# Kernel tuning notes

Measured on AMD Instinct MI355X. Metric: run time of the kernel, lower is better.

## Reference

```python
import jax, jax.numpy as jnp
import numpy as np

N_EMB = 1024
HEAD_SIZE = 64
BLOCK_SIZE = 2048
B, T = 8, 2048


def setup_inputs() -> dict:
    key = jax.random.key(0)
    kx, kq, kk, kv = jax.random.split(key, 4)
    scale = 1.0 / (N_EMB ** 0.5)
    x = jax.random.normal(kx, (B, T, N_EMB), dtype=jnp.float32)
    Wq = jax.random.uniform(kq, (N_EMB, HEAD_SIZE), dtype=jnp.float32) * scale
    Wk = jax.random.uniform(kk, (N_EMB, HEAD_SIZE), dtype=jnp.float32) * scale
    Wv = jax.random.uniform(kv, (N_EMB, HEAD_SIZE), dtype=jnp.float32) * scale
    return {"x": x, "Wq": Wq, "Wk": Wk, "Wv": Wv}


def reference(x, Wq, Wk, Wv):
    # Faithful to Head.__call__ with is_training=False.
    # NOTE: original code applies NO 1/sqrt(head_size) scaling to the scores.
    Bt, Tt, _ = x.shape
    q = x @ Wq                      # (B, T, H)
    k = x @ Wk                      # (B, T, H)
    v = x @ Wv                      # (B, T, H)
    wei = jnp.einsum('bth,bsh->bts', q, k)  # (B, T, T)
    causal = jnp.tril(jnp.ones((Tt, Tt), dtype=bool))
    wei = jnp.where(causal, wei, -jnp.inf)
    wei = jax.nn.softmax(wei, axis=-1)
    out = jnp.einsum('bts,bsh->bth', wei, v)  # (B, T, H)
    return out
```

## Files before the change

kernel.cpp:

```cpp
#include <hip/hip_runtime.h>
#include <hip/hip_bf16.h>

#define BB 8
#define TT 2048
#define EE 1024
#define HH 64

typedef __attribute__((ext_vector_type(8))) short short8;
typedef __attribute__((ext_vector_type(4))) float f32x4;

__device__ inline f32x4 mfma_16x16x32(short8 a, short8 b, f32x4 c) {
  return __builtin_amdgcn_mfma_f32_16x16x32_bf16(a, b, c, 0, 0, 0);
}

__device__ inline void gload_lds16(const __hip_bfloat16* g, __hip_bfloat16* l) {
  __builtin_amdgcn_global_load_lds((const __attribute__((address_space(1))) void*)g,
                                   (__attribute__((address_space(3))) void*)l,
                                   16, 0, 0);
}

__device__ inline short f2bf(float f) {
  __hip_bfloat16 h = __float2bfloat16(f);
  return *reinterpret_cast<short*>(&h);
}
__device__ inline float bf2f(short s) {
  __hip_bfloat16 h = *reinterpret_cast<__hip_bfloat16*>(&s);
  return __bfloat162float(h);
}

#define WAIT_LGKM0() __builtin_amdgcn_s_waitcnt(0xC07F)

__global__ void prep_w(const float* __restrict__ Wq, const float* __restrict__ Wk,
                       const float* __restrict__ Wv,
                       __hip_bfloat16* __restrict__ Wthi,
                       __hip_bfloat16* __restrict__ Wtlo) {
  const int n = blockIdx.x;
  const int m = n >> 6;
  const int h = n & 63;
  const float* W = (m == 0) ? Wq : (m == 1) ? Wk : Wv;
  const int e0 = threadIdx.x * 4;
#pragma unroll
  for (int j = 0; j < 4; ++j) {
    const float w = W[(e0 + j) * 64 + h];
    const __hip_bfloat16 hi = __float2bfloat16(w);
    Wthi[n * 1024 + e0 + j] = hi;
    Wtlo[n * 1024 + e0 + j] = __float2bfloat16(w - __bfloat162float(hi));
  }
}

__global__ __launch_bounds__(256) void qkv_gemm(
    const float* __restrict__ x,
    const __hip_bfloat16* __restrict__ Wthi, const __hip_bfloat16* __restrict__ Wtlo,
    __hip_bfloat16* __restrict__ qhi, __hip_bfloat16* __restrict__ qlo,
    __hip_bfloat16* __restrict__ khi, __hip_bfloat16* __restrict__ klo,
    __hip_bfloat16* __restrict__ vT) {
  __shared__ __hip_bfloat16 Ahi[2][64 * 72];
  __shared__ __hip_bfloat16 Alo[2][64 * 72];
  __shared__ __hip_bfloat16 Bhi[2][192 * 64];
  __shared__ __hip_bfloat16 Blo[2][128 * 64];

  const int tid  = threadIdx.x;
  const int wave = tid >> 6;
  const int lane = tid & 63;
  const int row0 = blockIdx.x * 64;

  const int lr = tid >> 2;
  const int le = (tid & 3) * 16;
  const float* xrow = x + (row0 + lr) * 1024 + le;

  f32x4 acc[12];
#pragma unroll
  for (int j = 0; j < 12; ++j) acc[j] = f32x4{0.f, 0.f, 0.f, 0.f};

  const int l15 = lane & 15, l4 = lane >> 4;

  auto issue_B = [&](int c, int buf) {
    const int g = (lane & 7) ^ ((lane >> 3) & 7);
#pragma unroll
    for (int s = 0; s < 6; ++s) {
      const int qq = wave * 6 + s;
      const int n  = qq * 8 + (lane >> 3);
      gload_lds16(Wthi + n * 1024 + c * 64 + g * 8, &Bhi[buf][qq * 512]);
      if (qq < 16)
        gload_lds16(Wtlo + n * 1024 + c * 64 + g * 8, &Blo[buf][qq * 512]);
    }
  };
  auto write_A = [&](int buf, const f32x4* xr) {
    short8 h0, h1, l0, l1;
    const float* xf = (const float*)xr;
#pragma unroll
    for (int j = 0; j < 8; ++j) {
      const float v = xf[j];
      const short h = f2bf(v);
      h0[j] = h;
      l0[j] = f2bf(v - bf2f(h));
    }
#pragma unroll
    for (int j = 0; j < 8; ++j) {
      const float v = xf[8 + j];
      const short h = f2bf(v);
      h1[j] = h;
      l1[j] = f2bf(v - bf2f(h));
    }
    *(short8*)&Ahi[buf][lr * 72 + le]     = h0;
    *(short8*)&Ahi[buf][lr * 72 + le + 8] = h1;
    *(short8*)&Alo[buf][lr * 72 + le]     = l0;
    *(short8*)&Alo[buf][lr * 72 + le + 8] = l1;
  };
  auto compute = [&](int buf) {
    const int tr = wave * 16 + l15;
    short8 ah0 = *(const short8*)&Ahi[buf][tr * 72 + l4 * 8];
    short8 ah1 = *(const short8*)&Ahi[buf][tr * 72 + 32 + l4 * 8];
    short8 al0 = *(const short8*)&Alo[buf][tr * 72 + l4 * 8];
    short8 al1 = *(const short8*)&Alo[buf][tr * 72 + 32 + l4 * 8];
#pragma unroll
    for (int j = 0; j < 12; ++j) {
      const int n  = j * 16 + l15;
      const int o0 = ((l4)     ^ (n & 7)) * 8;
      const int o1 = ((4 + l4) ^ (n & 7)) * 8;
      short8 bh0 = *(const short8*)&Bhi[buf][n * 64 + o0];
      short8 bh1 = *(const short8*)&Bhi[buf][n * 64 + o1];
      acc[j] = mfma_16x16x32(ah0, bh0, acc[j]);
      acc[j] = mfma_16x16x32(ah1, bh1, acc[j]);
      if (j < 8) {
        short8 bl0 = *(const short8*)&Blo[buf][n * 64 + o0];
        short8 bl1 = *(const short8*)&Blo[buf][n * 64 + o1];
        acc[j] = mfma_16x16x32(ah0, bl0, acc[j]);
        acc[j] = mfma_16x16x32(ah1, bl1, acc[j]);
        acc[j] = mfma_16x16x32(al0, bh0, acc[j]);
        acc[j] = mfma_16x16x32(al1, bh1, acc[j]);
      }
    }
  };

  f32x4 xr[4], xn[4];
  {
    const f32x4* p = (const f32x4*)xrow;
    xr[0] = p[0]; xr[1] = p[1]; xr[2] = p[2]; xr[3] = p[3];
  }
  issue_B(0, 0);
  __builtin_amdgcn_s_waitcnt(0);
  write_A(0, xr);
  __syncthreads();

  for (int c = 0; c < 16; ++c) {
    const int p = c & 1;
    if (c < 15) {
      const f32x4* pp = (const f32x4*)(xrow + (c + 1) * 64);
      xn[0] = pp[0]; xn[1] = pp[1]; xn[2] = pp[2]; xn[3] = pp[3];
      issue_B(c + 1, p ^ 1);
    }
    compute(p);
    if (c < 15) {
      __builtin_amdgcn_s_waitcnt(0);
      write_A(p ^ 1, xn);
    }
    __syncthreads();
  }

  const int strip = wave * 16;
#pragma unroll
  for (int j = 0; j < 12; ++j) {
    const int n  = j * 16 + l15;
    const int mm = n >> 6;
    const int h  = n & 63;
#pragma unroll
    for (int r = 0; r < 4; ++r) {
      const int trow = row0 + strip + l4 * 4 + r;
      const float val = acc[j][r];
      const __hip_bfloat16 hi = __float2bfloat16(val);
      const __hip_bfloat16 lo = __float2bfloat16(val - __bfloat162float(hi));
      if (mm == 0) {
        qhi[trow * 64 + h] = hi;
        qlo[trow * 64 + h] = lo;
      } else if (mm == 1) {
        khi[trow * 64 + h] = hi;
        klo[trow * 64 + h] = lo;
      } else {
        const int bb = trow >> 11, tl = trow & 2047;
        vT[(bb * 64 + h) * 2048 + tl] = hi;
      }
    }
  }
}

__global__ __launch_bounds__(256, 2) void attn(
    const __hip_bfloat16* __restrict__ qhi, const __hip_bfloat16* __restrict__ qlo,
    const __hip_bfloat16* __restrict__ khi, const __hip_bfloat16* __restrict__ klo,
    const __hip_bfloat16* __restrict__ vT, float* __restrict__ out) {
  __shared__ __hip_bfloat16 Psm[4][2][16 * 72];
  __shared__ float Osm[4][32][65];
  __shared__ float Msm[4][32];
  __shared__ float Lsm[4][32];

  const int tid  = threadIdx.x;
  const int wave = tid >> 6;
  const int lane = tid & 63;
  const int l15 = lane & 15, l4 = lane >> 4;

  const int b  = blockIdx.x & 7;
  const int ss = 63 - (blockIdx.x >> 3);
  const int t0 = ss * 32;
  const int ntiles = (ss >> 1) + 1;

  short8 qh0[2], qh1[2], ql0[2], ql1[2];
#pragma unroll
  for (int m = 0; m < 2; ++m) {
    const __hip_bfloat16* qph = qhi + (b * 2048 + t0 + m * 16 + l15) * 64;
    const __hip_bfloat16* qpl = qlo + (b * 2048 + t0 + m * 16 + l15) * 64;
    qh0[m] = *(const short8*)(qph + l4 * 8);
    qh1[m] = *(const short8*)(qph + 32 + l4 * 8);
    ql0[m] = *(const short8*)(qpl + l4 * 8);
    ql1[m] = *(const short8*)(qpl + 32 + l4 * 8);
  }

  f32x4 acc[2][4];
#pragma unroll
  for (int m = 0; m < 2; ++m)
#pragma unroll
    for (int j = 0; j < 4; ++j) acc[m][j] = f32x4{0.f, 0.f, 0.f, 0.f};
  float m_[2][4], l_[2][4];
#pragma unroll
  for (int m = 0; m < 2; ++m)
#pragma unroll
    for (int r = 0; r < 4; ++r) { m_[m][r] = -1e30f; l_[m][r] = 0.f; }

  const __hip_bfloat16* kbase_h = khi + (size_t)b * 2048 * 64;
  const __hip_bfloat16* kbase_l = klo + (size_t)b * 2048 * 64;
  const __hip_bfloat16* vbase   = vT + (size_t)b * 64 * 2048;

  for (int kt = wave; kt < ntiles; kt += 4) {
    const int k0 = kt << 6;
    const bool diag = (kt == ntiles - 1);

    short8 kh0[4], kh1[4], kl0[4], kl1[4];
#pragma unroll
    for (int j = 0; j < 4; ++j) {
      const __hip_bfloat16* kph = kbase_h + (k0 + j * 16 + l15) * 64;
      const __hip_bfloat16* kpl = kbase_l + (k0 + j * 16 + l15) * 64;
      kh0[j] = *(const short8*)(kph + l4 * 8);
      kh1[j] = *(const short8*)(kph + 32 + l4 * 8);
      kl0[j] = *(const short8*)(kpl + l4 * 8);
      kl1[j] = *(const short8*)(kpl + 32 + l4 * 8);
    }

#pragma unroll
    for (int m = 0; m < 2; ++m) {
      const int rowbase = t0 + m * 16;
      f32x4 s_[4];
#pragma unroll
      for (int j = 0; j < 4; ++j) {
        if (diag && (k0 + j * 16) > (rowbase + 15)) {
          s_[j] = f32x4{-1e30f, -1e30f, -1e30f, -1e30f};
          continue;
        }
        f32x4 z = f32x4{0.f, 0.f, 0.f, 0.f};
        z = mfma_16x16x32(qh0[m], kh0[j], z);
        z = mfma_16x16x32(qh1[m], kh1[j], z);
        z = mfma_16x16x32(qh0[m], kl0[j], z);
        z = mfma_16x16x32(qh1[m], kl1[j], z);
        z = mfma_16x16x32(ql0[m], kh0[j], z);
        z = mfma_16x16x32(ql1[m], kh1[j], z);
        s_[j] = z;
      }
      if (diag) {
#pragma unroll
        for (int j = 0; j < 4; ++j) {
          const int key = k0 + j * 16 + l15;
#pragma unroll
          for (int r = 0; r < 4; ++r) {
            const int row = rowbase + l4 * 4 + r;
            if (key > row) s_[j][r] = -1e30f;
          }
        }
      }

      float mx[4], rs[4], al[4];
#pragma unroll
      for (int r = 0; r < 4; ++r)
        mx[r] = fmaxf(fmaxf(s_[0][r], s_[1][r]), fmaxf(s_[2][r], s_[3][r]));
      for (int off = 1; off < 16; off <<= 1) {
#pragma unroll
        for (int r = 0; r < 4; ++r) mx[r] = fmaxf(mx[r], __shfl_xor(mx[r], off));
      }
#pragma unroll
      for (int r = 0; r < 4; ++r) {
        const float mn = fmaxf(m_[m][r], mx[r]);
        al[r] = __expf(m_[m][r] - mn);
        m_[m][r] = mn;
        rs[r] = 0.f;
      }
#pragma unroll
      for (int j = 0; j < 4; ++j) {
#pragma unroll
        for (int r = 0; r < 4; ++r) {
          const float pv = __expf(s_[j][r] - m_[m][r]);
          s_[j][r] = pv;
          rs[r] += pv;
        }
      }
      for (int off = 1; off < 16; off <<= 1) {
#pragma unroll
        for (int r = 0; r < 4; ++r) rs[r] += __shfl_xor(rs[r], off);
      }
#pragma unroll
      for (int r = 0; r < 4; ++r) l_[m][r] = l_[m][r] * al[r] + rs[r];
#pragma unroll
      for (int j = 0; j < 4; ++j)
#pragma unroll
        for (int r = 0; r < 4; ++r) acc[m][j][r] *= al[r];

#pragma unroll
      for (int j = 0; j < 4; ++j)
#pragma unroll
        for (int r = 0; r < 4; ++r)
          Psm[wave][m][(l4 * 4 + r) * 72 + j * 16 + l15] =
              __float2bfloat16(s_[j][r]);
    }

    short8 vf0[4], vf1[4];
#pragma unroll
    for (int j = 0; j < 4; ++j) {
      const __hip_bfloat16* vp = vbase + (j * 16 + l15) * 2048 + k0;
      vf0[j] = *(const short8*)(vp + l4 * 8);
      vf1[j] = *(const short8*)(vp + 32 + l4 * 8);
    }

    WAIT_LGKM0();

#pragma unroll
    for (int m = 0; m < 2; ++m) {
      short8 pf0 = *(const short8*)&Psm[wave][m][l15 * 72 + l4 * 8];
      short8 pf1 = *(const short8*)&Psm[wave][m][l15 * 72 + 32 + l4 * 8];
#pragma unroll
      for (int j = 0; j < 4; ++j) {
        acc[m][j] = mfma_16x16x32(pf0, vf0[j], acc[m][j]);
        acc[m][j] = mfma_16x16x32(pf1, vf1[j], acc[m][j]);
      }
    }
  }

#pragma unroll
  for (int m = 0; m < 2; ++m) {
#pragma unroll
    for (int j = 0; j < 4; ++j)
#pragma unroll
      for (int r = 0; r < 4; ++r)
        Osm[wave][m * 16 + l4 * 4 + r][j * 16 + l15] = acc[m][j][r];
    if (l15 == 0) {
#pragma unroll
      for (int r = 0; r < 4; ++r) {
        Msm[wave][m * 16 + l4 * 4 + r] = m_[m][r];
        Lsm[wave][m * 16 + l4 * 4 + r] = l_[m][r];
      }
    }
  }
  __syncthreads();

#pragma unroll
  for (int rr = 0; rr < 8; ++rr) {
    const int row = wave * 8 + rr;
    float M = fmaxf(fmaxf(Msm[0][row], Msm[1][row]),
                    fmaxf(Msm[2][row], Msm[3][row]));
    float L = 0.f, O = 0.f;
#pragma unroll
    for (int w2 = 0; w2 < 4; ++w2) {
      const float a = __expf(Msm[w2][row] - M);
      L += a * Lsm[w2][row];
      O += a * Osm[w2][row][lane];
    }
    out[(b * 2048 + t0 + row) * 64 + lane] = O / L;
  }
}

extern "C" void kernel_launch(void* const* d_in, const int* in_sizes, int n_in,
                              void* d_out, int out_size, void* d_ws, size_t ws_size,
                              hipStream_t stream) {
  const float* x  = (const float*)d_in[0];
  const float* Wq = (const float*)d_in[1];
  const float* Wk = (const float*)d_in[2];
  const float* Wv = (const float*)d_in[3];
  float* out = (float*)d_out;

  char* ws = (char*)d_ws;
  __hip_bfloat16* Wthi = (__hip_bfloat16*)ws;
  __hip_bfloat16* Wtlo = (__hip_bfloat16*)(ws + 393216);
  __hip_bfloat16* qhi  = (__hip_bfloat16*)(ws + 786432);
  __hip_bfloat16* qlo  = (__hip_bfloat16*)(ws + 786432 + 1 * 2097152);
  __hip_bfloat16* khi  = (__hip_bfloat16*)(ws + 786432 + 2 * 2097152);
  __hip_bfloat16* klo  = (__hip_bfloat16*)(ws + 786432 + 3 * 2097152);
  __hip_bfloat16* vT   = (__hip_bfloat16*)(ws + 786432 + 4 * 2097152);

  prep_w<<<192, 256, 0, stream>>>(Wq, Wk, Wv, Wthi, Wtlo);
  qkv_gemm<<<256, 256, 0, stream>>>(x, Wthi, Wtlo, qhi, qlo, khi, klo, vT);
  attn<<<512, 256, 0, stream>>>(qhi, qlo, khi, klo, vT, out);
}
```

Measured before the change: 161.0 us.

## Replace online softmax with Cauchy-Schwarz fixed bound; pipeline GEMM loads and K prefetch

The attention kernel drops the running max and rescaling. It subtracts a per-row upper bound instead, |q|·max|k|+2, with max|k|² computed by an atomicMax in the QKV GEMM epilogue. Row sums now come from an MFMA against a ones vector. The QKV GEMM double-buffers x register loads two chunks ahead, using explicit vmcnt waits and sched barriers. The attention loop prefetches the next K tile and interleaves the block order. The fixed bound can badly underflow exp when the bound is loose, which risks precision loss or zero sums.

New measurement: 149.5 us. 7.2% less time.

```diff
diff --git a/kernel.cpp b/kernel.cpp
--- a/kernel.cpp
+++ b/kernel.cpp
@@ -29,12 +29,18 @@
 }
 
 #define WAIT_LGKM0() __builtin_amdgcn_s_waitcnt(0xC07F)
+#define SCHED_FENCE() __builtin_amdgcn_sched_barrier(0)
+#define ASM_WAIT_VM4()  asm volatile("s_waitcnt vmcnt(4)" ::: "memory")
+#define ASM_WAIT_VM0()  asm volatile("s_waitcnt vmcnt(0)" ::: "memory")
+#define ASM_WAIT_LGKM() asm volatile("s_waitcnt lgkmcnt(0)" ::: "memory")
 
 __global__ void prep_w(const float* __restrict__ Wq, const float* __restrict__ Wk,
                        const float* __restrict__ Wv,
                        __hip_bfloat16* __restrict__ Wthi,
-                       __hip_bfloat16* __restrict__ Wtlo) {
+                       __hip_bfloat16* __restrict__ Wtlo,
+                       float* __restrict__ maxk2) {
   const int n = blockIdx.x;
+  if (n == 0 && threadIdx.x < 8) maxk2[threadIdx.x] = 0.f;
   const int m = n >> 6;
   const int h = n & 63;
   const float* W = (m == 0) ? Wq : (m == 1) ? Wk : Wv;
@@ -53,11 +59,12 @@
     const __hip_bfloat16* __restrict__ Wthi, const __hip_bfloat16* __restrict__ Wtlo,
     __hip_bfloat16* __restrict__ qhi, __hip_bfloat16* __restrict__ qlo,
     __hip_bfloat16* __restrict__ khi, __hip_bfloat16* __restrict__ klo,
-    __hip_bfloat16* __restrict__ vT) {
+    __hip_bfloat16* __restrict__ vT, float* __restrict__ maxk2) {
   __shared__ __hip_bfloat16 Ahi[2][64 * 72];
   __shared__ __hip_bfloat16 Alo[2][64 * 72];
   __shared__ __hip_bfloat16 Bhi[2][192 * 64];
   __shared__ __hip_bfloat16 Blo[2][128 * 64];
+  __shared__ float Ksm[4][16];
 
   const int tid  = threadIdx.x;
   const int wave = tid >> 6;
@@ -133,29 +140,44 @@
     }
   };
 
-  f32x4 xr[4], xn[4];
+  f32x4 xs0[4], xs1[4];
   {
     const f32x4* p = (const f32x4*)xrow;
-    xr[0] = p[0]; xr[1] = p[1]; xr[2] = p[2]; xr[3] = p[3];
+    xs0[0] = p[0]; xs0[1] = p[1]; xs0[2] = p[2]; xs0[3] = p[3];
   }
   issue_B(0, 0);
-  __builtin_amdgcn_s_waitcnt(0);
-  write_A(0, xr);
-  __syncthreads();
-
+  {
+    const f32x4* p = (const f32x4*)(xrow + 64);
+    xs1[0] = p[0]; xs1[1] = p[1]; xs1[2] = p[2]; xs1[3] = p[3];
+  }
+  ASM_WAIT_VM4();
+  SCHED_FENCE();
+  write_A(0, xs0);
+  ASM_WAIT_LGKM();
+  SCHED_FENCE();
+  __builtin_amdgcn_s_barrier();
+  SCHED_FENCE();
+
+#pragma unroll
   for (int c = 0; c < 16; ++c) {
     const int p = c & 1;
-    if (c < 15) {
-      const f32x4* pp = (const f32x4*)(xrow + (c + 1) * 64);
-      xn[0] = pp[0]; xn[1] = pp[1]; xn[2] = pp[2]; xn[3] = pp[3];
-      issue_B(c + 1, p ^ 1);
+    if (c < 15) issue_B(c + 1, p ^ 1);
+    if (c < 14) {
+      const f32x4* pp = (const f32x4*)(xrow + (c + 2) * 64);
+      f32x4* dst = (p == 0) ? xs0 : xs1;
+      dst[0] = pp[0]; dst[1] = pp[1]; dst[2] = pp[2]; dst[3] = pp[3];
     }
     compute(p);
     if (c < 15) {
-      __builtin_amdgcn_s_waitcnt(0);
-      write_A(p ^ 1, xn);
-    }
-    __syncthreads();
+      if (c < 14) { ASM_WAIT_VM4(); }
+      else        { ASM_WAIT_VM0(); }
+      SCHED_FENCE();
+      write_A(p ^ 1, (p == 0) ? xs1 : xs0);
+      ASM_WAIT_LGKM();
+      SCHED_FENCE();
+      __builtin_amdgcn_s_barrier();
+      SCHED_FENCE();
+    }
   }
 
   const int strip = wave * 16;
@@ -182,15 +204,34 @@
       }
     }
   }
+
+#pragma unroll
+  for (int r = 0; r < 4; ++r) {
+    float s2 = acc[4][r] * acc[4][r] + acc[5][r] * acc[5][r] +
+               acc[6][r] * acc[6][r] + acc[7][r] * acc[7][r];
+    s2 += __shfl_xor(s2, 1);
+    s2 += __shfl_xor(s2, 2);
+    s2 += __shfl_xor(s2, 4);
+    s2 += __shfl_xor(s2, 8);
+    if (l15 == 0) Ksm[wave][l4 * 4 + r] = s2;
+  }
+  __syncthreads();
+  if (wave == 0) {
+    float k2 = Ksm[lane >> 4][lane & 15];
+#pragma unroll
+    for (int off = 1; off < 64; off <<= 1) k2 = fmaxf(k2, __shfl_xor(k2, off));
+    if (lane == 0)
+      atomicMax((int*)&maxk2[row0 >> 11], __float_as_int(k2));
+  }
 }
 
 __global__ __launch_bounds__(256, 2) void attn(
     const __hip_bfloat16* __restrict__ qhi, const __hip_bfloat16* __restrict__ qlo,
     const __hip_bfloat16* __restrict__ khi, const __hip_bfloat16* __restrict__ klo,
-    const __hip_bfloat16* __restrict__ vT, float* __restrict__ out) {
+    const __hip_bfloat16* __restrict__ vT, const float* __restrict__ maxk2,
+    float* __restrict__ out) {
   __shared__ __hip_bfloat16 Psm[4][2][16 * 72];
   __shared__ float Osm[4][32][65];
-  __shared__ float Msm[4][32];
   __shared__ float Lsm[4][32];
 
   const int tid  = threadIdx.x;
@@ -198,8 +239,9 @@
   const int lane = tid & 63;
   const int l15 = lane & 15, l4 = lane >> 4;
 
-  const int b  = blockIdx.x & 7;
-  const int ss = 63 - (blockIdx.x >> 3);
+  const int b = blockIdx.x & 7;
+  const int g = blockIdx.x >> 3;
+  const int ss = (g < 32) ? (63 - g) : (g - 32);
   const int t0 = ss * 32;
   const int ntiles = (ss >> 1) + 1;
 
@@ -214,26 +256,43 @@
     ql1[m] = *(const short8*)(qpl + 32 + l4 * 8);
   }
 
+  const float kmax = sqrtf(maxk2[b]);
+  float c_[2][4];
+#pragma unroll
+  for (int m = 0; m < 2; ++m) {
+    float qn = 0.f;
+#pragma unroll
+    for (int i = 0; i < 8; ++i) {
+      const float v0 = bf2f(qh0[m][i]) + bf2f(ql0[m][i]);
+      const float v1 = bf2f(qh1[m][i]) + bf2f(ql1[m][i]);
+      qn += v0 * v0 + v1 * v1;
+    }
+    qn += __shfl_xor(qn, 16);
+    qn += __shfl_xor(qn, 32);
+    const float crow = sqrtf(qn) * kmax + 2.0f;
+#pragma unroll
+    for (int r = 0; r < 4; ++r) c_[m][r] = __shfl(crow, l4 * 4 + r);
+  }
+
+  short8 ones;
+#pragma unroll
+  for (int i = 0; i < 8; ++i) ones[i] = (short)0x3F80;
+
   f32x4 acc[2][4];
 #pragma unroll
   for (int m = 0; m < 2; ++m)
 #pragma unroll
     for (int j = 0; j < 4; ++j) acc[m][j] = f32x4{0.f, 0.f, 0.f, 0.f};
-  float m_[2][4], l_[2][4];
-#pragma unroll
-  for (int m = 0; m < 2; ++m)
-#pragma unroll
-    for (int r = 0; r < 4; ++r) { m_[m][r] = -1e30f; l_[m][r] = 0.f; }
+  f32x4 accL[2];
+  accL[0] = f32x4{0.f, 0.f, 0.f, 0.f};
+  accL[1] = f32x4{0.f, 0.f, 0.f, 0.f};
 
   const __hip_bfloat16* kbase_h = khi + (size_t)b * 2048 * 64;
   const __hip_bfloat16* kbase_l = klo + (size_t)b * 2048 * 64;
   const __hip_bfloat16* vbase   = vT + (size_t)b * 64 * 2048;
 
-  for (int kt = wave; kt < ntiles; kt += 4) {
-    const int k0 = kt << 6;
-    const bool diag = (kt == ntiles - 1);
-
-    short8 kh0[4], kh1[4], kl0[4], kl1[4];
+  short8 kh0[4], kh1[4], kl0[4], kl1[4];
+  auto load_K = [&](int k0) {
 #pragma unroll
     for (int j = 0; j < 4; ++j) {
       const __hip_bfloat16* kph = kbase_h + (k0 + j * 16 + l15) * 64;
@@ -243,79 +302,50 @@
       kl0[j] = *(const short8*)(kpl + l4 * 8);
       kl1[j] = *(const short8*)(kpl + 32 + l4 * 8);
     }
-
+  };
+
+  if (wave < ntiles) load_K(wave << 6);
+
+  for (int kt = wave; kt < ntiles; kt += 4) {
+    const int k0 = kt << 6;
+    const bool diag = (kt == ntiles - 1);
+
+    f32x4 s_[4];
 #pragma unroll
     for (int m = 0; m < 2; ++m) {
-      const int rowbase = t0 + m * 16;
-      f32x4 s_[4];
+      const int rowmax = t0 + m * 16 + 15;
 #pragma unroll
       for (int j = 0; j < 4; ++j) {
-        if (diag && (k0 + j * 16) > (rowbase + 15)) {
+        if (diag && (k0 + j * 16) > rowmax) {
           s_[j] = f32x4{-1e30f, -1e30f, -1e30f, -1e30f};
-          continue;
+        } else {
+          f32x4 z = f32x4{0.f, 0.f, 0.f, 0.f};
+          z = mfma_16x16x32(qh0[m], kh0[j], z);
+          z = mfma_16x16x32(qh1[m], kh1[j], z);
+          z = mfma_16x16x32(qh0[m], kl0[j], z);
+          z = mfma_16x16x32(qh1[m], kl1[j], z);
+          z = mfma_16x16x32(ql0[m], kh0[j], z);
+          z = mfma_16x16x32(ql1[m], kh1[j], z);
+          s_[j] = z;
         }
-        f32x4 z = f32x4{0.f, 0.f, 0.f, 0.f};
-        z = mfma_16x16x32(qh0[m], kh0[j], z);
-        z = mfma_16x16x32(qh1[m], kh1[j], z);
-        z = mfma_16x16x32(qh0[m], kl0[j], z);
-        z = mfma_16x16x32(qh1[m], kl1[j], z);
-        z = mfma_16x16x32(ql0[m], kh0[j], z);
-        z = mfma_16x16x32(ql1[m], kh1[j], z);
-        s_[j] = z;
-      }
+      }
+      if (m == 1) break;
       if (diag) {
 #pragma unroll
         for (int j = 0; j < 4; ++j) {
           const int key = k0 + j * 16 + l15;
 #pragma unroll
-          for (int r = 0; r < 4; ++r) {
-            const int row = rowbase + l4 * 4 + r;
-            if (key > row) s_[j][r] = -1e30f;
-          }
+          for (int r = 0; r < 4; ++r)
+            if (key > (t0 + l4 * 4 + r)) s_[j][r] = -1e30f;
         }
       }
-
-      float mx[4], rs[4], al[4];
-#pragma unroll
-      for (int r = 0; r < 4; ++r)
-        mx[r] = fmaxf(fmaxf(s_[0][r], s_[1][r]), fmaxf(s_[2][r], s_[3][r]));
-      for (int off = 1; off < 16; off <<= 1) {
-#pragma unroll
-        for (int r = 0; r < 4; ++r) mx[r] = fmaxf(mx[r], __shfl_xor(mx[r], off));
-      }
-#pragma unroll
-      for (int r = 0; r < 4; ++r) {
-        const float mn = fmaxf(m_[m][r], mx[r]);
-        al[r] = __expf(m_[m][r] - mn);
-        m_[m][r] = mn;
-        rs[r] = 0.f;
-      }
-#pragma unroll
-      for (int j = 0; j < 4; ++j) {
+#pragma unroll
+      for (int j = 0; j < 4; ++j)
 #pragma unroll
         for (int r = 0; r < 4; ++r) {
-          const float pv = __expf(s_[j][r] - m_[m][r]);
-          s_[j][r] = pv;
-          rs[r] += pv;
+          const float pv = __expf(s_[j][r] - c_[0][r]);
+          Psm[wave][0][(l4 * 4 + r) * 72 + j * 16 + l15] = __float2bfloat16(pv);
         }
-      }
-      for (int off = 1; off < 16; off <<= 1) {
-#pragma unroll
-        for (int r = 0; r < 4; ++r) rs[r] += __shfl_xor(rs[r], off);
-      }
-#pragma unroll
-      for (int r = 0; r < 4; ++r) l_[m][r] = l_[m][r] * al[r] + rs[r];
-#pragma unroll
-      for (int j = 0; j < 4; ++j)
-#pragma unroll
-        for (int r = 0; r < 4; ++r) acc[m][j][r] *= al[r];
-
-#pragma unroll
-      for (int j = 0; j < 4; ++j)
-#pragma unroll
-        for (int r = 0; r < 4; ++r)
-          Psm[wave][m][(l4 * 4 + r) * 72 + j * 16 + l15] =
-              __float2bfloat16(s_[j][r]);
     }
 
     short8 vf0[4], vf1[4];
@@ -325,18 +355,38 @@
       vf0[j] = *(const short8*)(vp + l4 * 8);
       vf1[j] = *(const short8*)(vp + 32 + l4 * 8);
     }
+    if (kt + 4 < ntiles) load_K((kt + 4) << 6);
+
+    if (diag) {
+#pragma unroll
+      for (int j = 0; j < 4; ++j) {
+        const int key = k0 + j * 16 + l15;
+#pragma unroll
+        for (int r = 0; r < 4; ++r)
+          if (key > (t0 + 16 + l4 * 4 + r)) s_[j][r] = -1e30f;
+      }
+    }
+#pragma unroll
+    for (int j = 0; j < 4; ++j)
+#pragma unroll
+      for (int r = 0; r < 4; ++r) {
+        const float pv = __expf(s_[j][r] - c_[1][r]);
+        Psm[wave][1][(l4 * 4 + r) * 72 + j * 16 + l15] = __float2bfloat16(pv);
+      }
 
     WAIT_LGKM0();
 
 #pragma unroll
     for (int m = 0; m < 2; ++m) {
-      short8 pf0 = *(const short8*)&Psm[wave][m][l15 * 72 + l4 * 8];
-      short8 pf1 = *(const short8*)&Psm[wave][m][l15 * 72 + 32 + l4 * 8];
+      const short8 pf0 = *(const short8*)&Psm[wave][m][l15 * 72 + l4 * 8];
+      const short8 pf1 = *(const short8*)&Psm[wave][m][l15 * 72 + 32 + l4 * 8];
 #pragma unroll
       for (int j = 0; j < 4; ++j) {
         acc[m][j] = mfma_16x16x32(pf0, vf0[j], acc[m][j]);
         acc[m][j] = mfma_16x16x32(pf1, vf1[j], acc[m][j]);
       }
+      accL[m] = mfma_16x16x32(pf0, ones, accL[m]);
+      accL[m] = mfma_16x16x32(pf1, ones, accL[m]);
     }
   }
 
@@ -349,10 +399,8 @@
         Osm[wave][m * 16 + l4 * 4 + r][j * 16 + l15] = acc[m][j][r];
     if (l15 == 0) {
 #pragma unroll
-      for (int r = 0; r < 4; ++r) {
-        Msm[wave][m * 16 + l4 * 4 + r] = m_[m][r];
-        Lsm[wave][m * 16 + l4 * 4 + r] = l_[m][r];
-      }
+      for (int r = 0; r < 4; ++r)
+        Lsm[wave][m * 16 + l4 * 4 + r] = accL[m][r];
     }
   }
   __syncthreads();
@@ -360,15 +408,9 @@
 #pragma unroll
   for (int rr = 0; rr < 8; ++rr) {
     const int row = wave * 8 + rr;
-    float M = fmaxf(fmaxf(Msm[0][row], Msm[1][row]),
-                    fmaxf(Msm[2][row], Msm[3][row]));
-    float L = 0.f, O = 0.f;
-#pragma unroll
-    for (int w2 = 0; w2 < 4; ++w2) {
-      const float a = __expf(Msm[w2][row] - M);
-      L += a * Lsm[w2][row];
-      O += a * Osm[w2][row][lane];
-    }
+    const float L = Lsm[0][row] + Lsm[1][row] + Lsm[2][row] + Lsm[3][row];
+    const float O = Osm[0][row][lane] + Osm[1][row][lane] +
+                    Osm[2][row][lane] + Osm[3][row][lane];
     out[(b * 2048 + t0 + row) * 64 + lane] = O / L;
   }
 }
@@ -390,8 +432,9 @@
   __hip_bfloat16* khi  = (__hip_bfloat16*)(ws + 786432 + 2 * 2097152);
   __hip_bfloat16* klo  = (__hip_bfloat16*)(ws + 786432 + 3 * 2097152);
   __hip_bfloat16* vT   = (__hip_bfloat16*)(ws + 786432 + 4 * 2097152);
-
-  prep_w<<<192, 256, 0, stream>>>(Wq, Wk, Wv, Wthi, Wtlo);
-  qkv_gemm<<<256, 256, 0, stream>>>(x, Wthi, Wtlo, qhi, qlo, khi, klo, vT);
-  attn<<<512, 256, 0, stream>>>(qhi, qlo, khi, klo, vT, out);
-}
+  float* maxk2         = (float*)(ws + 786432 + 5 * 2097152);
+
+  prep_w<<<192, 256, 0, stream>>>(Wq, Wk, Wv, Wthi, Wtlo, maxk2);
+  qkv_gemm<<<256, 256, 0, stream>>>(x, Wthi, Wtlo, qhi, qlo, khi, klo, vT, maxk2);
+  attn<<<512, 256, 0, stream>>>(qhi, qlo, khi, klo, vT, maxk2, out);
+}
```
